# Kernel optimization log

Hardware: AMD Instinct MI355X
Metric: run time of the kernel (lower is better)

Reference implementation:

```python
import jax, jax.numpy as jnp
import numpy as np

E = 8      # num_experts
R = 32     # LoRA rank
D = 1024   # in_features (d_model)
H = 4096   # out_features of fc1 (hidden)
B = 2
S = 2048
SCALING = 1.0 / R  # lora_alpha / rank with alpha=1


def setup_inputs() -> dict:
    key = jax.random.key(0)
    ks = jax.random.split(key, 9)
    def w(k, shape, scale=0.02):
        return jax.random.normal(k, shape, dtype=jnp.float32) * scale
    return {
        "x": jax.random.normal(ks[0], (B, S, D), dtype=jnp.float32),
        "router_w": w(ks[1], (E, D)),
        "router_b": jnp.zeros((E,), jnp.float32),
        "fc1_w": w(ks[2], (H, D)),
        "fc1_b": jnp.zeros((H,), jnp.float32),
        "fc2_w": w(ks[3], (D, H)),
        "fc2_b": jnp.zeros((D,), jnp.float32),
        "A_down": w(ks[4], (E, R, D)),
        "Ab_down": jnp.zeros((E, R), jnp.float32),
        "B_down": w(ks[5], (E, H, R)),
        "Bb_down": jnp.zeros((E, H), jnp.float32),
        "A_up": w(ks[6], (E, R, H)),
        "Ab_up": jnp.zeros((E, R), jnp.float32),
        "B_up": w(ks[7], (E, D, R)),
        "Bb_up": jnp.zeros((E, D), jnp.float32),
    }


def _moe_lora(x, mask, A, Ab, Bw, Bb):
    # x: [B,S,din]; mask: one-hot [B,S,E]; A: [E,R,din]; Bw: [E,dout,R]
    # rank-stage for all experts is cheap (R=32), select per token via one-hot
    h = jnp.einsum('bsd,erd->bser', x, A) + Ab          # [B,S,E,R]
    hsel = jnp.einsum('bser,bse->bsr', h, mask)          # [B,S,R]
    out = jnp.zeros(x.shape[:2] + (Bw.shape[1],), dtype=x.dtype)
    for e in range(E):  # fixed small expert count; avoids [B,S,E,dout] blowup
        out = out + mask[..., e:e + 1] * (hsel @ Bw[e].T + Bb[e])
    return out * SCALING


def reference(x, router_w, router_b, fc1_w, fc1_b, fc2_w, fc2_b,
              A_down, Ab_down, B_down, Bb_down,
              A_up, Ab_up, B_up, Bb_up):
    logits = x @ router_w.T + router_b                   # [B,S,E]
    routing = jax.nn.softmax(logits, axis=-1)
    index = jnp.argmax(logits, axis=-1)                  # top-1 expert [B,S]
    mask = jax.nn.one_hot(index, E, dtype=x.dtype)       # y_hard [B,S,E]
    expert_choice = mask - jax.lax.stop_gradient(routing) + routing
    # down: frozen fc1 + sparse LoRA (dropout layers in eval mode -> identity)
    down = x @ fc1_w.T + fc1_b + _moe_lora(x, mask, A_down, Ab_down, B_down, Bb_down)
    a = jax.nn.gelu(down, approximate=False)             # F.gelu exact
    up = a @ fc2_w.T + fc2_b + _moe_lora(a, mask, A_up, Ab_up, B_up, Bb_up)
    return up, routing, expert_choice
```

## Files before the change

kernel.cpp:

```cpp
#include <hip/hip_runtime.h>
#include <hip/hip_bf16.h>
#include <math.h>
#include <stdint.h>

#define E_ 8
#define R_ 32
#define D_ 1024
#define H_ 4096
#define NTOK 4096
#define M_MAX 5120
#define TILES_MAX 40
#define SCALING 0.03125f

typedef __attribute__((ext_vector_type(8))) __bf16 bf16x8;
typedef __attribute__((ext_vector_type(8))) unsigned short ushort8;
typedef __attribute__((ext_vector_type(4))) float floatx4;

__device__ __forceinline__ unsigned short f2b(float f) {
    union { float f; unsigned int i; } v; v.f = f;
    unsigned int x = v.i;
    x += 0x7fffu + ((x >> 16) & 1u);
    return (unsigned short)(x >> 16);
}
__device__ __forceinline__ float gelu_fast(float v) {
    float u = v * (0.7978845608028654f + 0.0356774080857f * v * v);
    float t = __expf(-2.f * fabsf(u));
    float th = (1.f - t) * __builtin_amdgcn_rcpf(1.f + t);
    th = (u >= 0.f) ? th : -th;
    return 0.5f * v * (1.f + th);
}

#define GLOAD_LDS16(g, l) __builtin_amdgcn_global_load_lds( \
    (const __attribute__((address_space(1))) void*)(g),     \
    (__attribute__((address_space(3))) void*)(l), 16, 0, 0)

__global__ __launch_bounds__(256) void k_prep(
    const float* __restrict__ w1, const float* __restrict__ w2,
    const float* __restrict__ Ad, const float* __restrict__ Bd,
    const float* __restrict__ Au, const float* __restrict__ Bu,
    unsigned short* __restrict__ w1b, unsigned short* __restrict__ w2b,
    unsigned short* __restrict__ Adb, unsigned short* __restrict__ Bdb,
    unsigned short* __restrict__ Aub, unsigned short* __restrict__ Bub,
    const float* __restrict__ x, const float* __restrict__ rw,
    const float* __restrict__ rb,
    float* __restrict__ out, int* __restrict__ idx)
{
    if (blockIdx.x < 5376) {
        long g = ((long)blockIdx.x * 256 + threadIdx.x) * 8;
        const float* src; unsigned short* dst; long off;
        if      (g <  4194304L) { src = w1; dst = w1b; off = 0; }
        else if (g <  8388608L) { src = w2; dst = w2b; off = 4194304L; }
        else if (g <  8650752L) { src = Ad; dst = Adb; off = 8388608L; }
        else if (g <  9699328L) { src = Bd; dst = Bdb; off = 8650752L; }
        else if (g < 10747904L) { src = Au; dst = Aub; off = 9699328L; }
        else                    { src = Bu; dst = Bub; off = 10747904L; }
        long i = g - off;
        float4 a = *(const float4*)(src + i);
        float4 b = *(const float4*)(src + i + 4);
        ushort8 o;
        o[0] = f2b(a.x); o[1] = f2b(a.y); o[2] = f2b(a.z); o[3] = f2b(a.w);
        o[4] = f2b(b.x); o[5] = f2b(b.y); o[6] = f2b(b.z); o[7] = f2b(b.w);
        *(ushort8*)(dst + i) = o;
        return;
    }
    const int wave = threadIdx.x >> 6, lane = threadIdx.x & 63;
    const int t = (blockIdx.x - 5376) * 4 + wave;
    const float4* xr = (const float4*)(x + (size_t)t * D_);
    float4 xv[4];
#pragma unroll
    for (int s = 0; s < 4; ++s) xv[s] = xr[lane + 64 * s];
    float acc[E_];
#pragma unroll
    for (int e = 0; e < E_; ++e) {
        const float4* wr = (const float4*)(rw + (size_t)e * D_);
        float s = 0.f;
#pragma unroll
        for (int u = 0; u < 4; ++u) {
            float4 wv = wr[lane + 64 * u];
            s += xv[u].x * wv.x + xv[u].y * wv.y + xv[u].z * wv.z + xv[u].w * wv.w;
        }
        acc[e] = s;
    }
#pragma unroll
    for (int e = 0; e < E_; ++e) {
#pragma unroll
        for (int m = 32; m > 0; m >>= 1) acc[e] += __shfl_xor(acc[e], m, 64);
        acc[e] += rb[e];
    }
    int best = 0;
#pragma unroll
    for (int e = 1; e < E_; ++e) if (acc[e] > acc[best]) best = e;
    const float mx = acc[best];
    float pr[E_]; float se = 0.f;
#pragma unroll
    for (int e = 0; e < E_; ++e) { pr[e] = expf(acc[e] - mx); se += pr[e]; }
    const float inv = 1.f / se;
    if (lane < E_) {
        float r = pr[lane] * inv;
        out[(size_t)NTOK * D_ + (size_t)t * E_ + lane] = r;
        float maskv = (lane == best) ? 1.f : 0.f;
        out[(size_t)NTOK * D_ + (size_t)NTOK * E_ + (size_t)t * E_ + lane] = (maskv - r) + r;
    }
    if (lane == 0) idx[t] = best;
}

__global__ __launch_bounds__(256) void k_scan(
    const int* __restrict__ idx, int* __restrict__ hdr,
    int* __restrict__ tile_e, int* __restrict__ gather)
{
    __shared__ int cnt[256][E_];
    __shared__ int tot[E_], base[E_];
    const int tid = threadIdx.x;
    for (int m = tid; m < M_MAX; m += 256) gather[m] = -1;
    int c[E_];
#pragma unroll
    for (int e = 0; e < E_; ++e) c[e] = 0;
    for (int t = tid * 16; t < tid * 16 + 16; ++t) c[idx[t] & 7]++;
#pragma unroll
    for (int e = 0; e < E_; ++e) cnt[tid][e] = c[e];
    __syncthreads();
    if (tid < E_) {
        int run = 0;
        for (int i = 0; i < 256; ++i) { int v = cnt[i][tid]; cnt[i][tid] = run; run += v; }
        tot[tid] = run;
    }
    __syncthreads();
    if (tid == 0) {
        int b = 0, tp = 0;
        for (int e = 0; e < E_; ++e) {
            base[e] = b;
            int nt = (tot[e] + 127) >> 7;
            for (int k = 0; k < nt; ++k) tile_e[tp++] = e;
            b += nt << 7;
        }
        hdr[0] = b;
        hdr[1] = tp;
        for (int k = tp; k < TILES_MAX; ++k) tile_e[k] = 0;
    }
    __syncthreads();
    int p[E_];
#pragma unroll
    for (int e = 0; e < E_; ++e) p[e] = base[e] + cnt[tid][e];
    for (int t = tid * 16; t < tid * 16 + 16; ++t) { int e = idx[t] & 7; gather[p[e]++] = t; }
}

__global__ __launch_bounds__(128) void k_gather(
    const float* __restrict__ x, const int* __restrict__ gather,
    unsigned short* __restrict__ xg)
{
    const int m = blockIdx.x, tid = threadIdx.x;
    const int t = gather[m];
    ushort8* dst = (ushort8*)(xg + (size_t)m * D_);
    ushort8 o;
    if ((unsigned)t < (unsigned)NTOK) {
        const float4* src = (const float4*)(x + (size_t)t * D_);
        float4 a = src[tid * 2], b = src[tid * 2 + 1];
        o[0] = f2b(a.x); o[1] = f2b(a.y); o[2] = f2b(a.z); o[3] = f2b(a.w);
        o[4] = f2b(b.x); o[5] = f2b(b.y); o[6] = f2b(b.z); o[7] = f2b(b.w);
    } else {
        o = (ushort8)(0);
    }
    dst[tid] = o;
}

__global__ __launch_bounds__(256) void k_lora_a2(
    const unsigned short* __restrict__ A,
    const unsigned short* __restrict__ W,
    const float* __restrict__ Ab,
    const int* __restrict__ hdr, const int* __restrict__ tile_e,
    unsigned short* __restrict__ outb,
    int Ktot)
{
    const int mtile = blockIdx.y;
    int ntiles = hdr[1]; if (ntiles > TILES_MAX) ntiles = TILES_MAX;
    if (mtile >= ntiles) return;
    const int e = tile_e[mtile] & 7;
    const int m0 = mtile * 128 + blockIdx.x * 32;
    const int wave = threadIdx.x >> 6, lane = threadIdx.x & 63;
    const int q = lane >> 4, l16 = lane & 15;
    const int Ks = Ktot >> 2;
    const int kbase = wave * Ks;
    const floatx4 z4 = {0.f, 0.f, 0.f, 0.f};
    floatx4 acc[2][2] = {{z4, z4}, {z4, z4}};
    const bf16x8* A0 = (const bf16x8*)(A + (size_t)(m0 + l16) * Ktot);
    const bf16x8* A1 = (const bf16x8*)(A + (size_t)(m0 + 16 + l16) * Ktot);
    const bf16x8* W0 = (const bf16x8*)(W + ((size_t)e * 32 + l16) * Ktot);
    const bf16x8* W1 = (const bf16x8*)(W + ((size_t)e * 32 + 16 + l16) * Ktot);
    for (int k = kbase; k < kbase + Ks; k += 32) {
        int u = (k >> 3) + q;
        bf16x8 a0 = A0[u], a1 = A1[u];
        bf16x8 b0 = W0[u], b1 = W1[u];
        acc[0][0] = __builtin_amdgcn_mfma_f32_16x16x32_bf16(a0, b0, acc[0][0], 0, 0, 0);
        acc[0][1] = __builtin_amdgcn_mfma_f32_16x16x32_bf16(a0, b1, acc[0][1], 0, 0, 0);
        acc[1][0] = __builtin_amdgcn_mfma_f32_16x16x32_bf16(a1, b0, acc[1][0], 0, 0, 0);
        acc[1][1] = __builtin_amdgcn_mfma_f32_16x16x32_bf16(a1, b1, acc[1][1], 0, 0, 0);
    }
    __shared__ float red[4][32][32];
#pragma unroll
    for (int mi = 0; mi < 2; ++mi)
#pragma unroll
        for (int ni = 0; ni < 2; ++ni)
#pragma unroll
            for (int r = 0; r < 4; ++r)
                red[wave][mi * 16 + q * 4 + r][ni * 16 + l16] = acc[mi][ni][r];
    __syncthreads();
    for (int i = threadIdx.x; i < 1024; i += 256) {
        int lr = i >> 5, c = i & 31;
        float s = red[0][lr][c] + red[1][lr][c] + red[2][lr][c] + red[3][lr][c];
        outb[(size_t)(m0 + lr) * 32 + c] = f2b(SCALING * (s + Ab[e * 32 + c]));
    }
}

#define STG_H0(S2, KO) do { \
    GLOAD_LDS16(Ar + (KO),                         As3 + (S2) * 2048 +        wave * 64); \
    GLOAD_LDS16(Ar + (size_t)64  * KTOT + (KO),    As3 + (S2) * 2048 +  512 + wave * 64); \
    GLOAD_LDS16(Br + (KO),                         Bs3 + (S2) * 1024 +        wave * 64); \
} while (0)
#define STG_H1(S2, KO) do { \
    GLOAD_LDS16(Ar + (size_t)128 * KTOT + (KO),    As3 + (S2) * 2048 + 1024 + wave * 64); \
    GLOAD_LDS16(Ar + (size_t)192 * KTOT + (KO),    As3 + (S2) * 2048 + 1536 + wave * 64); \
    GLOAD_LDS16(Br + (size_t)64  * KTOT + (KO),    Bs3 + (S2) * 1024 +  512 + wave * 64); \
} while (0)

template <int KTOT, bool IS_FC1, int NSPLIT>
__global__ __launch_bounds__(512, 2) void k_mlp8(
    const unsigned short* __restrict__ Amat,
    const unsigned short* __restrict__ Wmat,
    const float* __restrict__ bias,
    const unsigned short* __restrict__ lora_h,
    const unsigned short* __restrict__ lora_B,
    const float* __restrict__ lora_b,
    const int* __restrict__ hdr, const int* __restrict__ tile_e,
    const int* __restrict__ gather,
    unsigned short* __restrict__ outb,
    float* __restrict__ outf,
    float* __restrict__ P,
    int NOUT)
{
    constexpr int NT = (KTOT / NSPLIT) / 64;
    int nt128 = hdr[1]; if (nt128 > TILES_MAX) nt128 = TILES_MAX;
    const int n256 = (nt128 + 1) >> 1;
    const int NXB = (int)gridDim.x;
    const int NYB = (int)gridDim.y;
    const int nwg = NXB * NYB;
    const int lid = (int)blockIdx.x + NXB * (int)blockIdx.y;
    const int tlin = (lid & 7) * (nwg >> 3) + (lid >> 3);
    const int mt2 = tlin % NYB;
    const int tx  = tlin / NYB;
    if (mt2 >= n256) return;
    const int m0 = mt2 * 256;
    const int h0 = tx * 128;
    const int kstart = (NSPLIT > 1) ? (int)blockIdx.z * (KTOT / NSPLIT) : 0;

    __shared__ bf16x8 As3[6144];
    __shared__ bf16x8 Bs3[3072];

    const int tid  = threadIdx.x;
    const int wave = tid >> 6, lane = tid & 63;
    const int l16 = lane & 15, q = lane >> 4;
    const int wm = wave & 3, wn = wave >> 2;
    const int idx0 = q ^ (l16 & 7);
    const int arow = wm * 64 + l16;
    const int brow = wn * 64 + l16;
    const int rrow = tid >> 3;
    const int jj8  = (((tid & 7) ^ (rrow & 7)) << 3);
    const unsigned short* Abase = Amat + (size_t)m0 * KTOT + kstart;
    const unsigned short* Bbase = Wmat + (size_t)h0 * KTOT + kstart;
    const unsigned short* Ar = Abase + (size_t)rrow * KTOT + jj8;
    const unsigned short* Br = Bbase + (size_t)rrow * KTOT + jj8;

    const floatx4 z4 = {0.f, 0.f, 0.f, 0.f};
    floatx4 acc[4][4];
#pragma unroll
    for (int mi = 0; mi < 4; ++mi)
#pragma unroll
        for (int ni = 0; ni < 4; ++ni) acc[mi][ni] = z4;

    STG_H0(0, 0);  STG_H1(0, 0);
    STG_H0(1, 64); STG_H1(1, 64);
    asm volatile("s_waitcnt vmcnt(6)" ::: "memory");
    __builtin_amdgcn_s_barrier();

    int slot = 0, slot2 = 2;
#pragma unroll 1
    for (int kt = 0; kt < NT; ++kt) {
        const int sA = slot << 11, sB = slot << 10;
        const int ko2 = (kt + 2) << 6;
        const bool more = (kt + 2) < NT;
        bf16x8 af[4], bfr[4], ag2[4], bg2[4];
#pragma unroll
        for (int mi = 0; mi < 4; ++mi) af[mi]  = As3[sA + ((arow + mi * 16) << 3) + idx0];
#pragma unroll
        for (int ni = 0; ni < 4; ++ni) bfr[ni] = Bs3[sB + ((brow + ni * 16) << 3) + idx0];
        if (more) STG_H0(slot2, ko2);
        __builtin_amdgcn_s_setprio(1);
#pragma unroll
        for (int mi = 0; mi < 4; ++mi)
#pragma unroll
            for (int ni = 0; ni < 4; ++ni)
                acc[mi][ni] = __builtin_amdgcn_mfma_f32_16x16x32_bf16(af[mi], bfr[ni], acc[mi][ni], 0, 0, 0);
        __builtin_amdgcn_s_setprio(0);
#pragma unroll
        for (int mi = 0; mi < 4; ++mi) ag2[mi] = As3[sA + ((arow + mi * 16) << 3) + (idx0 ^ 4)];
#pragma unroll
        for (int ni = 0; ni < 4; ++ni) bg2[ni] = Bs3[sB + ((brow + ni * 16) << 3) + (idx0 ^ 4)];
        if (more) {
            STG_H1(slot2, ko2);
            asm volatile("s_waitcnt vmcnt(6)" ::: "memory");
        } else {
            asm volatile("s_waitcnt vmcnt(0)" ::: "memory");
        }
        __builtin_amdgcn_s_setprio(1);
#pragma unroll
        for (int mi = 0; mi < 4; ++mi)
#pragma unroll
            for (int ni = 0; ni < 4; ++ni)
                acc[mi][ni] = __builtin_amdgcn_mfma_f32_16x16x32_bf16(ag2[mi], bg2[ni], acc[mi][ni], 0, 0, 0);
        __builtin_amdgcn_s_setprio(0);
        __builtin_amdgcn_s_barrier();
        slot  = (slot  == 2) ? 0 : slot  + 1;
        slot2 = (slot2 == 2) ? 0 : slot2 + 1;
    }

    const bool extras = (NSPLIT == 1) || (blockIdx.z == 0);
    const int e = tile_e[(mt2 << 1) + (wm >> 1)] & 7;
    if (extras) {
        bf16x8 a2[4], b2[4];
#pragma unroll
        for (int mi = 0; mi < 4; ++mi)
            a2[mi] = *(const bf16x8*)(lora_h + (size_t)(m0 + wm * 64 + mi * 16 + l16) * 32 + q * 8);
#pragma unroll
        for (int ni = 0; ni < 4; ++ni)
            b2[ni] = *(const bf16x8*)(lora_B + ((size_t)e * NOUT + h0 + wn * 64 + ni * 16 + l16) * 32 + q * 8);
#pragma unroll
        for (int mi = 0; mi < 4; ++mi)
#pragma unroll
            for (int ni = 0; ni < 4; ++ni)
                acc[mi][ni] = __builtin_amdgcn_mfma_f32_16x16x32_bf16(a2[mi], b2[ni], acc[mi][ni], 0, 0, 0);
    }

#pragma unroll
    for (int ni = 0; ni < 4; ++ni) {
        const int gh = h0 + wn * 64 + ni * 16 + l16;
        const float bv = extras ? (bias[gh] + SCALING * lora_b[e * NOUT + gh]) : 0.f;
#pragma unroll
        for (int mi = 0; mi < 4; ++mi) {
#pragma unroll
            for (int r = 0; r < 4; ++r) {
                const int gm = m0 + wm * 64 + mi * 16 + q * 4 + r;
                const float v = acc[mi][ni][r] + bv;
                if (IS_FC1) {
                    outb[(size_t)gm * NOUT + gh] = f2b(gelu_fast(v));
                } else if (extras) {
                    const int t = gather[gm];
                    if ((unsigned)t < (unsigned)NTOK) outf[(size_t)t * NOUT + gh] = v;
                } else {
                    P[(size_t)gm * NOUT + gh] = v;
                }
            }
        }
    }
}

__global__ __launch_bounds__(256) void k_reduce(
    const float* __restrict__ P, const int* __restrict__ gather,
    float* __restrict__ out)
{
    const int m = blockIdx.x;
    const int t = gather[m];
    if ((unsigned)t >= (unsigned)NTOK) return;
    const float4* p4 = (const float4*)(P + (size_t)m * D_);
    float4* o4 = (float4*)(out + (size_t)t * D_);
    int i = threadIdx.x;
    float4 a = o4[i], b = p4[i];
    a.x += b.x; a.y += b.y; a.z += b.z; a.w += b.w;
    o4[i] = a;
}

#define OFF_IDX      0u
#define OFF_HDR      16384u
#define OFF_TILE     16640u
#define OFF_GATHER   16896u
#define OFF_XG       37376u
#define OFF_W1B      10523136u
#define OFF_ADB      18911744u
#define OFF_BDB      19436032u
#define OFF_HSB      21533184u
#define OFF_P        37376u
#define OFF_AG       21860864u
#define OFF_HUB      63803904u
#define OFF_W2B      64131584u
#define OFF_AUB      72520192u
#define OFF_BUB      74617344u
#define WS_NEEDED    75141632u

extern "C" void kernel_launch(void* const* d_in, const int* in_sizes, int n_in,
                              void* d_out, int out_size, void* d_ws, size_t ws_size,
                              hipStream_t stream)
{
    (void)out_size;
    if (ws_size < (size_t)WS_NEEDED) return;
    if (n_in < 15 || in_sizes[0] != NTOK * D_ || in_sizes[3] != H_ * D_ ||
        in_sizes[5] != D_ * H_ || in_sizes[9] != E_ * H_ * R_) return;

    const float* x   = (const float*)d_in[0];
    const float* rw  = (const float*)d_in[1];
    const float* rb  = (const float*)d_in[2];
    const float* w1  = (const float*)d_in[3];
    const float* b1  = (const float*)d_in[4];
    const float* w2  = (const float*)d_in[5];
    const float* b2  = (const float*)d_in[6];
    const float* Ad  = (const float*)d_in[7];
    const float* Abd = (const float*)d_in[8];
    const float* Bd  = (const float*)d_in[9];
    const float* Bbd = (const float*)d_in[10];
    const float* Au  = (const float*)d_in[11];
    const float* Abu = (const float*)d_in[12];
    const float* Bu  = (const float*)d_in[13];
    const float* Bbu = (const float*)d_in[14];
    float* out = (float*)d_out;
    char* ws = (char*)d_ws;

    int* idx            = (int*)(ws + OFF_IDX);
    int* hdr            = (int*)(ws + OFF_HDR);
    int* tile_e         = (int*)(ws + OFF_TILE);
    int* gather         = (int*)(ws + OFF_GATHER);
    unsigned short* xg  = (unsigned short*)(ws + OFF_XG);
    unsigned short* hsb = (unsigned short*)(ws + OFF_HSB);
    unsigned short* ag  = (unsigned short*)(ws + OFF_AG);
    unsigned short* hub = (unsigned short*)(ws + OFF_HUB);
    unsigned short* w1b = (unsigned short*)(ws + OFF_W1B);
    unsigned short* w2b = (unsigned short*)(ws + OFF_W2B);
    unsigned short* Adb = (unsigned short*)(ws + OFF_ADB);
    unsigned short* Bdb = (unsigned short*)(ws + OFF_BDB);
    unsigned short* Aub = (unsigned short*)(ws + OFF_AUB);
    unsigned short* Bub = (unsigned short*)(ws + OFF_BUB);
    float* P            = (float*)(ws + OFF_P);

    k_prep<<<6400, 256, 0, stream>>>(w1, w2, Ad, Bd, Au, Bu,
                                     w1b, w2b, Adb, Bdb, Aub, Bub,
                                     x, rw, rb, out, idx);
    k_scan<<<1, 256, 0, stream>>>(idx, hdr, tile_e, gather);
    k_gather<<<M_MAX, 128, 0, stream>>>(x, gather, xg);
    k_lora_a2<<<dim3(4, TILES_MAX), 256, 0, stream>>>(xg, Adb, Abd, hdr, tile_e, hsb, D_);
    k_mlp8<D_, true, 1><<<dim3(H_ / 128, TILES_MAX / 2, 1), 512, 0, stream>>>(
        xg, w1b, b1, hsb, Bdb, Bbd, hdr, tile_e, gather, ag, nullptr, nullptr, H_);
    k_lora_a2<<<dim3(4, TILES_MAX), 256, 0, stream>>>(ag, Aub, Abu, hdr, tile_e, hub, H_);
    k_mlp8<H_, false, 2><<<dim3(D_ / 128, TILES_MAX / 2, 2), 512, 0, stream>>>(
        ag, w2b, b2, hub, Bub, Bbu, hdr, tile_e, gather, nullptr, out, P, D_);
    k_reduce<<<M_MAX, 256, 0, stream>>>(P, gather, out);
}
```

Before: 312.5 us.

## Enlarge grouped GEMM tile to 256x256 with double-buffered four-phase staging

The fused MLP GEMM tile grows from 256x128 to 256x256. Each wave now computes 128x64 (8x4 MFMA accumulators), which cuts global and LDS traffic per FLOP. Staging moves from a triple-buffered two-phase pipeline to a double-buffered scheme. All LDS fragments are read up front and the next tile's loads are interleaved in four MFMA phases separated by barriers. The cost is more accumulator registers (128 floats per lane), extra barriers, and half as many workgroups. That may lower occupancy and hurt load balance, especially for fc2 with only 4 column blocks.

New measurement: 338.1 us. +8.2%, slower.

```diff
diff --git a/kernel.cpp b/kernel.cpp
--- a/kernel.cpp
+++ b/kernel.cpp
@@ -211,19 +211,17 @@
     }
 }
 
-#define STG_H0(S2, KO) do { \
-    GLOAD_LDS16(Ar + (KO),                         As3 + (S2) * 2048 +        wave * 64); \
-    GLOAD_LDS16(Ar + (size_t)64  * KTOT + (KO),    As3 + (S2) * 2048 +  512 + wave * 64); \
-    GLOAD_LDS16(Br + (KO),                         Bs3 + (S2) * 1024 +        wave * 64); \
+#define STG_A(U, KO) do { \
+    GLOAD_LDS16(Ar + (size_t)((U) * 128)      * KTOT + (KO), As3 + bufo + (U) * 1024 +       wave * 64); \
+    GLOAD_LDS16(Ar + (size_t)((U) * 128 + 64) * KTOT + (KO), As3 + bufo + (U) * 1024 + 512 + wave * 64); \
 } while (0)
-#define STG_H1(S2, KO) do { \
-    GLOAD_LDS16(Ar + (size_t)128 * KTOT + (KO),    As3 + (S2) * 2048 + 1024 + wave * 64); \
-    GLOAD_LDS16(Ar + (size_t)192 * KTOT + (KO),    As3 + (S2) * 2048 + 1536 + wave * 64); \
-    GLOAD_LDS16(Br + (size_t)64  * KTOT + (KO),    Bs3 + (S2) * 1024 +  512 + wave * 64); \
+#define STG_B(U, KO) do { \
+    GLOAD_LDS16(Br + (size_t)((U) * 128)      * KTOT + (KO), Bs3 + bufo + (U) * 1024 +       wave * 64); \
+    GLOAD_LDS16(Br + (size_t)((U) * 128 + 64) * KTOT + (KO), Bs3 + bufo + (U) * 1024 + 512 + wave * 64); \
 } while (0)
 
 template <int KTOT, bool IS_FC1, int NSPLIT>
-__global__ __launch_bounds__(512, 2) void k_mlp8(
+__global__ __launch_bounds__(512, 2) void k_mlp10(
     const unsigned short* __restrict__ Amat,
     const unsigned short* __restrict__ Wmat,
     const float* __restrict__ bias,
@@ -249,18 +247,18 @@
     const int tx  = tlin / NYB;
     if (mt2 >= n256) return;
     const int m0 = mt2 * 256;
-    const int h0 = tx * 128;
+    const int h0 = tx * 256;
     const int kstart = (NSPLIT > 1) ? (int)blockIdx.z * (KTOT / NSPLIT) : 0;
 
-    __shared__ bf16x8 As3[6144];
-    __shared__ bf16x8 Bs3[3072];
+    __shared__ bf16x8 As3[4096];
+    __shared__ bf16x8 Bs3[4096];
 
     const int tid  = threadIdx.x;
     const int wave = tid >> 6, lane = tid & 63;
     const int l16 = lane & 15, q = lane >> 4;
-    const int wm = wave & 3, wn = wave >> 2;
+    const int wm = wave & 1, wn = wave >> 1;
     const int idx0 = q ^ (l16 & 7);
-    const int arow = wm * 64 + l16;
+    const int arow = wm * 128 + l16;
     const int brow = wn * 64 + l16;
     const int rrow = tid >> 3;
     const int jj8  = (((tid & 7) ^ (rrow & 7)) << 3);
@@ -270,70 +268,95 @@
     const unsigned short* Br = Bbase + (size_t)rrow * KTOT + jj8;
 
     const floatx4 z4 = {0.f, 0.f, 0.f, 0.f};
-    floatx4 acc[4][4];
-#pragma unroll
-    for (int mi = 0; mi < 4; ++mi)
+    floatx4 acc[8][4];
+#pragma unroll
+    for (int mi = 0; mi < 8; ++mi)
 #pragma unroll
         for (int ni = 0; ni < 4; ++ni) acc[mi][ni] = z4;
 
-    STG_H0(0, 0);  STG_H1(0, 0);
-    STG_H0(1, 64); STG_H1(1, 64);
+    {
+        int bufo = 0;
+        STG_A(0, 0); STG_A(1, 0); STG_B(0, 0); STG_B(1, 0);
+        bufo = 2048;
+        STG_A(0, 64); STG_A(1, 64); STG_B(0, 64); STG_B(1, 64);
+    }
     asm volatile("s_waitcnt vmcnt(6)" ::: "memory");
     __builtin_amdgcn_s_barrier();
 
-    int slot = 0, slot2 = 2;
+    int buf = 0;
 #pragma unroll 1
     for (int kt = 0; kt < NT; ++kt) {
-        const int sA = slot << 11, sB = slot << 10;
+        const int bufo = buf << 11;
         const int ko2 = (kt + 2) << 6;
         const bool more = (kt + 2) < NT;
-        bf16x8 af[4], bfr[4], ag2[4], bg2[4];
-#pragma unroll
-        for (int mi = 0; mi < 4; ++mi) af[mi]  = As3[sA + ((arow + mi * 16) << 3) + idx0];
-#pragma unroll
-        for (int ni = 0; ni < 4; ++ni) bfr[ni] = Bs3[sB + ((brow + ni * 16) << 3) + idx0];
-        if (more) STG_H0(slot2, ko2);
+        bf16x8 af[8][2], bfv[4][2];
+#pragma unroll
+        for (int mi = 0; mi < 8; ++mi) {
+            const int rb8 = bufo + ((arow + mi * 16) << 3);
+            af[mi][0] = As3[rb8 + idx0];
+            af[mi][1] = As3[rb8 + (idx0 ^ 4)];
+        }
+#pragma unroll
+        for (int ni = 0; ni < 4; ++ni) {
+            const int rb8 = bufo + ((brow + ni * 16) << 3);
+            bfv[ni][0] = Bs3[rb8 + idx0];
+            bfv[ni][1] = Bs3[rb8 + (idx0 ^ 4)];
+        }
+        asm volatile("s_waitcnt lgkmcnt(0)" ::: "memory");
+        __builtin_amdgcn_s_barrier();
+        if (more) STG_A(0, ko2);
         __builtin_amdgcn_s_setprio(1);
 #pragma unroll
         for (int mi = 0; mi < 4; ++mi)
 #pragma unroll
             for (int ni = 0; ni < 4; ++ni)
-                acc[mi][ni] = __builtin_amdgcn_mfma_f32_16x16x32_bf16(af[mi], bfr[ni], acc[mi][ni], 0, 0, 0);
-        __builtin_amdgcn_s_setprio(0);
-#pragma unroll
-        for (int mi = 0; mi < 4; ++mi) ag2[mi] = As3[sA + ((arow + mi * 16) << 3) + (idx0 ^ 4)];
-#pragma unroll
-        for (int ni = 0; ni < 4; ++ni) bg2[ni] = Bs3[sB + ((brow + ni * 16) << 3) + (idx0 ^ 4)];
-        if (more) {
-            STG_H1(slot2, ko2);
-            asm volatile("s_waitcnt vmcnt(6)" ::: "memory");
-        } else {
-            asm volatile("s_waitcnt vmcnt(0)" ::: "memory");
-        }
-        __builtin_amdgcn_s_setprio(1);
-#pragma unroll
-        for (int mi = 0; mi < 4; ++mi)
-#pragma unroll
-            for (int ni = 0; ni < 4; ++ni)
-                acc[mi][ni] = __builtin_amdgcn_mfma_f32_16x16x32_bf16(ag2[mi], bg2[ni], acc[mi][ni], 0, 0, 0);
+                acc[mi][ni] = __builtin_amdgcn_mfma_f32_16x16x32_bf16(af[mi][0], bfv[ni][0], acc[mi][ni], 0, 0, 0);
         __builtin_amdgcn_s_setprio(0);
         __builtin_amdgcn_s_barrier();
-        slot  = (slot  == 2) ? 0 : slot  + 1;
-        slot2 = (slot2 == 2) ? 0 : slot2 + 1;
+        if (more) STG_A(1, ko2);
+        __builtin_amdgcn_s_setprio(1);
+#pragma unroll
+        for (int mi = 4; mi < 8; ++mi)
+#pragma unroll
+            for (int ni = 0; ni < 4; ++ni)
+                acc[mi][ni] = __builtin_amdgcn_mfma_f32_16x16x32_bf16(af[mi][0], bfv[ni][0], acc[mi][ni], 0, 0, 0);
+        __builtin_amdgcn_s_setprio(0);
+        __builtin_amdgcn_s_barrier();
+        if (more) STG_B(0, ko2);
+        __builtin_amdgcn_s_setprio(1);
+#pragma unroll
+        for (int mi = 0; mi < 4; ++mi)
+#pragma unroll
+            for (int ni = 0; ni < 4; ++ni)
+                acc[mi][ni] = __builtin_amdgcn_mfma_f32_16x16x32_bf16(af[mi][1], bfv[ni][1], acc[mi][ni], 0, 0, 0);
+        __builtin_amdgcn_s_setprio(0);
+        __builtin_amdgcn_s_barrier();
+        if (more) STG_B(1, ko2);
+        __builtin_amdgcn_s_setprio(1);
+#pragma unroll
+        for (int mi = 4; mi < 8; ++mi)
+#pragma unroll
+            for (int ni = 0; ni < 4; ++ni)
+                acc[mi][ni] = __builtin_amdgcn_mfma_f32_16x16x32_bf16(af[mi][1], bfv[ni][1], acc[mi][ni], 0, 0, 0);
+        __builtin_amdgcn_s_setprio(0);
+        if (more) asm volatile("s_waitcnt vmcnt(6)" ::: "memory");
+        else      asm volatile("s_waitcnt vmcnt(0)" ::: "memory");
+        __builtin_amdgcn_s_barrier();
+        buf ^= 1;
     }
 
     const bool extras = (NSPLIT == 1) || (blockIdx.z == 0);
-    const int e = tile_e[(mt2 << 1) + (wm >> 1)] & 7;
+    const int e = tile_e[(mt2 << 1) + wm] & 7;
     if (extras) {
-        bf16x8 a2[4], b2[4];
-#pragma unroll
-        for (int mi = 0; mi < 4; ++mi)
-            a2[mi] = *(const bf16x8*)(lora_h + (size_t)(m0 + wm * 64 + mi * 16 + l16) * 32 + q * 8);
+        bf16x8 a2[8], b2[4];
+#pragma unroll
+        for (int mi = 0; mi < 8; ++mi)
+            a2[mi] = *(const bf16x8*)(lora_h + (size_t)(m0 + wm * 128 + mi * 16 + l16) * 32 + q * 8);
 #pragma unroll
         for (int ni = 0; ni < 4; ++ni)
             b2[ni] = *(const bf16x8*)(lora_B + ((size_t)e * NOUT + h0 + wn * 64 + ni * 16 + l16) * 32 + q * 8);
 #pragma unroll
-        for (int mi = 0; mi < 4; ++mi)
+        for (int mi = 0; mi < 8; ++mi)
 #pragma unroll
             for (int ni = 0; ni < 4; ++ni)
                 acc[mi][ni] = __builtin_amdgcn_mfma_f32_16x16x32_bf16(a2[mi], b2[ni], acc[mi][ni], 0, 0, 0);
@@ -344,10 +367,11 @@
         const int gh = h0 + wn * 64 + ni * 16 + l16;
         const float bv = extras ? (bias[gh] + SCALING * lora_b[e * NOUT + gh]) : 0.f;
 #pragma unroll
-        for (int mi = 0; mi < 4; ++mi) {
+        for (int mi = 0; mi < 8; ++mi) {
+            const int gmb = m0 + wm * 128 + mi * 16 + q * 4;
 #pragma unroll
             for (int r = 0; r < 4; ++r) {
-                const int gm = m0 + wm * 64 + mi * 16 + q * 4 + r;
+                const int gm = gmb + r;
                 const float v = acc[mi][ni][r] + bv;
                 if (IS_FC1) {
                     outb[(size_t)gm * NOUT + gh] = f2b(gelu_fast(v));
@@ -443,10 +467,10 @@
     k_scan<<<1, 256, 0, stream>>>(idx, hdr, tile_e, gather);
     k_gather<<<M_MAX, 128, 0, stream>>>(x, gather, xg);
     k_lora_a2<<<dim3(4, TILES_MAX), 256, 0, stream>>>(xg, Adb, Abd, hdr, tile_e, hsb, D_);
-    k_mlp8<D_, true, 1><<<dim3(H_ / 128, TILES_MAX / 2, 1), 512, 0, stream>>>(
+    k_mlp10<D_, true, 1><<<dim3(H_ / 256, TILES_MAX / 2, 1), 512, 0, stream>>>(
         xg, w1b, b1, hsb, Bdb, Bbd, hdr, tile_e, gather, ag, nullptr, nullptr, H_);
     k_lora_a2<<<dim3(4, TILES_MAX), 256, 0, stream>>>(ag, Aub, Abu, hdr, tile_e, hub, H_);
-    k_mlp8<H_, false, 2><<<dim3(D_ / 128, TILES_MAX / 2, 2), 512, 0, stream>>>(
+    k_mlp10<H_, false, 2><<<dim3(D_ / 256, TILES_MAX / 2, 2), 512, 0, stream>>>(
         ag, w2b, b2, hub, Bub, Bbu, hdr, tile_e, gather, nullptr, out, P, D_);
     k_reduce<<<M_MAX, 256, 0, stream>>>(P, gather, out);
 }
```
